# Kernel tuning notes

Measured on AMD Instinct MI355X. Metric: run time of the kernel, lower is better.

Reference implementation:

```python
import jax, jax.numpy as jnp
import numpy as np

DIM = 1024
HEADS = 16
HEAD_DIM = DIM // HEADS
BLOCK = 32
FEAT = 128
EPS = 1e-8


def setup_inputs() -> dict:
    key = jax.random.key(0)
    ks = jax.random.split(key, 5)
    b, n = 4, 4096
    x = jax.random.normal(ks[0], (b, n, DIM), dtype=jnp.float32)
    Wqkv = jax.random.normal(ks[1], (DIM, 3 * DIM), dtype=jnp.float32) / np.sqrt(DIM)
    proj = jax.random.normal(ks[2], (HEADS, HEAD_DIM, FEAT), dtype=jnp.float32) / np.sqrt(HEAD_DIM)
    Wout = jax.random.normal(ks[3], (DIM, DIM), dtype=jnp.float32) / np.sqrt(DIM)
    bout = jnp.zeros((DIM,), dtype=jnp.float32)
    return {"x": x, "Wqkv": Wqkv, "proj": proj, "Wout": Wout, "bout": bout}


def reference(x, Wqkv, proj, Wout, bout):
    b, n, d = x.shape
    h, dh = HEADS, HEAD_DIM
    nb = n // BLOCK
    qkv = x @ Wqkv                                    # [b, n, 3d]
    q, k, v = jnp.split(qkv, 3, axis=-1)
    # [b, h, nb, bs, dh]
    def to_blocks(t):
        return t.reshape(b, nb, BLOCK, h, dh).transpose(0, 3, 1, 2, 4)
    q, k, v = to_blocks(q), to_blocks(k), to_blocks(v)
    # per-head feature projection + elu feature map
    qf = jax.nn.elu(jnp.einsum('bhmsd,hdf->bhmsf', q, proj)) + 1.0
    kf = jax.nn.elu(jnp.einsum('bhmsd,hdf->bhmsf', k, proj)) + 1.0
    kv = jnp.einsum('bhmsf,bhmsd->bhmfd', kf, v)      # per-block kv state
    out = jnp.einsum('bhmsf,bhmfd->bhmsd', qf, kv)
    z = 1.0 / (jnp.einsum('bhmsf,bhmf->bhms', qf, kf.sum(axis=3)) + EPS)
    out = out * z[..., None]
    out = out.transpose(0, 2, 3, 1, 4).reshape(b, n, d)  # [b, n, d]
    return out @ Wout + bout
```

## Files before the change

### kernel.cpp

```cpp
#include <hip/hip_runtime.h>
#include <stdint.h>


typedef unsigned short u16;
typedef __attribute__((ext_vector_type(4))) float f32x4;
typedef __attribute__((ext_vector_type(8))) __bf16 bf16x8;
typedef __attribute__((ext_vector_type(8))) u16 us8;
typedef __attribute__((ext_vector_type(4))) u16 us4;

#define GLOAD_LDS16(g, l)                                                      \
  __builtin_amdgcn_global_load_lds(                                            \
      (const __attribute__((address_space(1))) void*)(g),                      \
      (__attribute__((address_space(3))) void*)(l), 16, 0, 0)

__device__ __forceinline__ u16 f2bf(float f) {
  union { float f; unsigned u; } x; x.f = f;
  return (u16)((x.u + 0x7fffu + ((x.u >> 16) & 1u)) >> 16);
}

__device__ __forceinline__ bf16x8 ld8(const void* p) {
  return __builtin_bit_cast(bf16x8, *(const us8*)p);
}

__device__ __forceinline__ f32x4 mfma16(bf16x8 a, bf16x8 b, f32x4 c) {
  return __builtin_amdgcn_mfma_f32_16x16x32_bf16(a, b, c, 0, 0, 0);
}

__global__ void cast_bf16_k(const float* __restrict__ in, u16* __restrict__ out,
                            int n4) {
  int stride = gridDim.x * blockDim.x;
  for (int i = blockIdx.x * blockDim.x + threadIdx.x; i < n4; i += stride) {
    f32x4 v = ((const f32x4*)in)[i];
    us4 o;
    o[0] = f2bf(v[0]); o[1] = f2bf(v[1]); o[2] = f2bf(v[2]); o[3] = f2bf(v[3]);
    ((us4*)out)[i] = o;
  }
}

__global__ __launch_bounds__(256)
void tcast_k(const float* __restrict__ in, u16* __restrict__ out, int R, int C) {
  __shared__ float tile[32][33];
  int tx = threadIdx.x & 31, ty = threadIdx.x >> 5;
  int r0 = blockIdx.y * 32, c0 = blockIdx.x * 32;
#pragma unroll
  for (int i = 0; i < 32; i += 8)
    tile[ty + i][tx] = in[(size_t)(r0 + ty + i) * C + c0 + tx];
  __syncthreads();
#pragma unroll
  for (int i = 0; i < 32; i += 8)
    out[(size_t)(c0 + ty + i) * R + r0 + tx] = f2bf(tile[tx][ty + i]);
}

__global__ __launch_bounds__(256)
void tcastv_k(const float* __restrict__ Wqkv, u16* __restrict__ dst) {
  __shared__ float tile[32][33];
  int tx = threadIdx.x & 31, ty = threadIdx.x >> 5;
  int e0 = blockIdx.y * 32, j0 = blockIdx.x * 32;
#pragma unroll
  for (int i = 0; i < 32; i += 8)
    tile[ty + i][tx] = Wqkv[(size_t)(e0 + ty + i) * 3072 + 2048 + j0 + tx];
  __syncthreads();
#pragma unroll
  for (int i = 0; i < 32; i += 8)
    dst[(size_t)(j0 + ty + i) * 1024 + e0 + tx] = f2bf(tile[tx][ty + i]);
}

__global__ __launch_bounds__(256)
void wqpb_k(const float* __restrict__ Wqkv, const float* __restrict__ proj,
            u16* __restrict__ Bt) {
  __shared__ float pl[64][128];
  const int ec = blockIdx.x, h = blockIdx.y, qk = blockIdx.z;
  const float* ph = proj + (size_t)h * 8192;
  for (int i = threadIdx.x; i < 2048; i += 256)
    ((f32x4*)&pl[0][0])[i] = ((const f32x4*)ph)[i];
  __syncthreads();
  const int e = ec * 128 + (threadIdx.x >> 1);
  const int f0 = (threadIdx.x & 1) * 64;
  float wrow[64];
  const float* src = Wqkv + (size_t)e * 3072 + qk * 1024 + h * 64;
#pragma unroll
  for (int i = 0; i < 16; ++i)
    *(f32x4*)&wrow[i * 4] = *(const f32x4*)&src[i * 4];
  u16* dst = Bt + (size_t)(h * 256 + qk * 128) * 1024 + e;
  for (int fg = 0; fg < 16; ++fg) {
    f32x4 acc = (f32x4){0.f, 0.f, 0.f, 0.f};
    const int f = f0 + fg * 4;
#pragma unroll
    for (int d = 0; d < 64; ++d) {
      f32x4 p = *(f32x4*)&pl[d][f];
      acc += wrow[d] * p;
    }
#pragma unroll
    for (int u = 0; u < 4; ++u) dst[(size_t)(f + u) * 1024] = f2bf(acc[u]);
  }
}

template <int EPI>
__global__ __launch_bounds__(512, 1)
void gemm8p_k(const u16* __restrict__ A, int lda,
              const u16* __restrict__ Bt, int ldb,
              const float* __restrict__ bias,
              u16* __restrict__ o_bf16, const u16* __restrict__ v_in,
              float* __restrict__ o_f32, int K, int ntx) {
  __shared__ __align__(16) char lds[131072];
  const int tid = threadIdx.x, lane = tid & 63, w = tid >> 6;
  const int wm = w >> 2, wn = w & 3;
  const int lr = lane & 15, lg = lane >> 4;
  const int cpx = (int)gridDim.x >> 3;
  const int bid = blockIdx.x;
  const int s = (bid & 7) * cpx + (bid >> 3);
  const int bxN = (s % ntx) * 256;
  const int byM = (s / ntx) * 256;
  const int nt = K >> 6;

  const int srow = w * 8 + (lane >> 3);
  const int scol = ((lane & 7) ^ ((lane >> 3) & 7)) * 8;

  auto stg = [&](const u16* src, int ld, int row0, int kt, int dstoff) {
#pragma unroll
    for (int j = 0; j < 2; ++j)
      GLOAD_LDS16(src + (size_t)(row0 + j * 64 + srow) * ld + kt + scol,
                  lds + dstoff + j * 8192 + w * 1024);
  };
  auto stgA0 = [&](int t) { stg(A, lda, byM, t * 64, (t & 1) * 65536); };
  auto stgA1 = [&](int t) { stg(A, lda, byM + 128, t * 64, (t & 1) * 65536 + 16384); };
  auto stgB0 = [&](int t) { stg(Bt, ldb, bxN, t * 64, (t & 1) * 65536 + 32768); };
  auto stgB1 = [&](int t) { stg(Bt, ldb, bxN + 128, t * 64, (t & 1) * 65536 + 49152); };

  f32x4 acc[8][4];
#pragma unroll
  for (int i = 0; i < 8; ++i)
#pragma unroll
    for (int j = 0; j < 4; ++j) acc[i][j] = (f32x4){0.f, 0.f, 0.f, 0.f};

  stgA0(0); stgA1(0); stgB0(0); stgB1(0);
  if (nt > 1) {
    stgB0(1); stgB1(1);
    asm volatile("s_waitcnt vmcnt(4)" ::: "memory");
  } else {
    asm volatile("s_waitcnt vmcnt(0)" ::: "memory");
  }
  __builtin_amdgcn_s_barrier();

  for (int t = 0; t < nt; ++t) {
    const char* Ab = lds + (t & 1) * 65536 + wm * 16384;
    const char* Bb = lds + (t & 1) * 65536 + 32768 + (wn >> 1) * 16384;
    const int brow = (wn & 1) * 64;
    bf16x8 alo[4][2], ahi[4][2], bl[4][2];

    if (t + 1 < nt) { stgA0(t + 1); stgA1(t + 1); }
#pragma unroll
    for (int i = 0; i < 4; ++i)
#pragma unroll
      for (int ks = 0; ks < 2; ++ks) {
        int row = i * 16 + lr;
        alo[i][ks] = ld8(Ab + row * 128 + ((ks * 64 + lg * 16) ^ ((row & 7) << 4)));
      }
#pragma unroll
    for (int j = 0; j < 4; ++j)
#pragma unroll
      for (int ks = 0; ks < 2; ++ks) {
        int row = brow + j * 16 + lr;
        bl[j][ks] = ld8(Bb + row * 128 + ((ks * 64 + lg * 16) ^ ((row & 7) << 4)));
      }
#pragma unroll
    for (int i = 0; i < 4; ++i)
#pragma unroll
      for (int j = 0; j < 4; ++j)
#pragma unroll
        for (int ks = 0; ks < 2; ++ks)
          acc[i][j] = mfma16(alo[i][ks], bl[j][ks], acc[i][j]);
    __builtin_amdgcn_s_barrier();

    if (t + 2 < nt) { stgB0(t + 2); stgB1(t + 2); }
#pragma unroll
    for (int i = 0; i < 4; ++i)
#pragma unroll
      for (int ks = 0; ks < 2; ++ks) {
        int row = (4 + i) * 16 + lr;
        ahi[i][ks] = ld8(Ab + row * 128 + ((ks * 64 + lg * 16) ^ ((row & 7) << 4)));
      }
#pragma unroll
    for (int i = 0; i < 4; ++i)
#pragma unroll
      for (int j = 0; j < 4; ++j)
#pragma unroll
        for (int ks = 0; ks < 2; ++ks)
          acc[4 + i][j] = mfma16(ahi[i][ks], bl[j][ks], acc[4 + i][j]);
    if (t < nt - 2)
      asm volatile("s_waitcnt vmcnt(4)" ::: "memory");
    else
      asm volatile("s_waitcnt vmcnt(0)" ::: "memory");
    __builtin_amdgcn_s_barrier();
  }

  if (EPI == 1) {
#pragma unroll
    for (int mi = 0; mi < 8; ++mi)
#pragma unroll
      for (int nj = 0; nj < 4; ++nj) {
        const int col = bxN + wn * 64 + nj * 16 + lr;
        const float bia = bias[col];
#pragma unroll
        for (int rr = 0; rr < 4; ++rr) {
          const int row = byM + wm * 128 + mi * 16 + lg * 4 + rr;
          o_f32[(size_t)row * 1024 + col] = acc[mi][nj][rr] + bia;
        }
      }
    return;
  }

  const int hh = bxN >> 8;

  us8 vreg[4];
  if (EPI == 0) {
    const u16* vrow = v_in +
        (size_t)(byM + w * 32 + (lane >> 1)) * 1024 + hh * 64 + (lane & 1) * 32;
#pragma unroll
    for (int c = 0; c < 4; ++c) vreg[c] = *(const us8*)&vrow[c * 8];
  }

  u16* cl = (u16*)lds;
#pragma unroll
  for (int mi = 0; mi < 8; ++mi)
#pragma unroll
    for (int nj = 0; nj < 4; ++nj)
#pragma unroll
      for (int rr = 0; rr < 4; ++rr) {
        const int rl = wm * 128 + mi * 16 + lg * 4 + rr;
        const int clm = wn * 64 + nj * 16 + lr;
        float xv = acc[mi][nj][rr];
        float v = (EPI == 0) ? (xv > 0.f ? xv + 1.f : __expf(xv)) : xv;
        *(u16*)((char*)cl + ((rl * 512 + clm * 2) ^ ((rl & 7) << 4))) = f2bf(v);
      }
  __syncthreads();

  if (EPI == 2) {
#pragma unroll
    for (int it = 0; it < 16; ++it) {
      const int chunk = it * 512 + tid;
      const int r = chunk >> 5, k = chunk & 31;
      us8 val = *(us8*)((char*)cl + ((r * 512 + k * 16) ^ ((r & 7) << 4)));
      *(us8*)&o_bf16[(size_t)(byM + r) * 1024 + bxN + k * 8] = val;
    }
    return;
  }

  char* sw = (char*)lds + w * 16384;

  f32x4 sacc[2][2];
#pragma unroll
  for (int mm = 0; mm < 2; ++mm)
#pragma unroll
    for (int nn = 0; nn < 2; ++nn) sacc[mm][nn] = (f32x4){0.f, 0.f, 0.f, 0.f};
#pragma unroll
  for (int ks = 0; ks < 4; ++ks) {
    bf16x8 aq[2], bk[2];
#pragma unroll
    for (int mm = 0; mm < 2; ++mm) {
      const int row = mm * 16 + lr;
      aq[mm] = ld8(sw + ((row * 512 + ks * 64 + lg * 16) ^ ((row & 7) << 4)));
      bk[mm] = ld8(sw + ((row * 512 + 256 + ks * 64 + lg * 16) ^ ((row & 7) << 4)));
    }
#pragma unroll
    for (int mm = 0; mm < 2; ++mm)
#pragma unroll
      for (int nn = 0; nn < 2; ++nn)
        sacc[mm][nn] = mfma16(aq[mm], bk[nn], sacc[mm][nn]);
  }

  float rs[2][4];
#pragma unroll
  for (int mm = 0; mm < 2; ++mm)
#pragma unroll
    for (int r = 0; r < 4; ++r) {
      float tv = sacc[mm][0][r] + sacc[mm][1][r];
      tv += __shfl_xor(tv, 1);
      tv += __shfl_xor(tv, 2);
      tv += __shfl_xor(tv, 4);
      tv += __shfl_xor(tv, 8);
      rs[mm][r] = tv;
    }

#pragma unroll
  for (int mm = 0; mm < 2; ++mm)
#pragma unroll
    for (int nn = 0; nn < 2; ++nn)
#pragma unroll
      for (int r = 0; r < 4; ++r) {
        const int row = mm * 16 + lg * 4 + r;
        *(u16*)(sw + row * 64 + (((nn * 16 + lr) * 2) ^ ((row & 3) << 4))) =
            f2bf(sacc[mm][nn][r]);
      }

#pragma unroll
  for (int c = 0; c < 4; ++c)
    *(us8*)(sw + 2048 + (lane >> 1) * 144 + (lane & 1) * 64 + c * 16) = vreg[c];
  const u16* V_l = (const u16*)(sw + 2048);
  bf16x8 vfr[4];
#pragma unroll
  for (int nn = 0; nn < 4; ++nn) {
    us8 g;
#pragma unroll
    for (int j = 0; j < 8; ++j) g[j] = V_l[(lg * 8 + j) * 72 + nn * 16 + lr];
    vfr[nn] = __builtin_bit_cast(bf16x8, g);
  }

  f32x4 pacc[2][4];
#pragma unroll
  for (int mm = 0; mm < 2; ++mm)
#pragma unroll
    for (int nn = 0; nn < 4; ++nn) pacc[mm][nn] = (f32x4){0.f, 0.f, 0.f, 0.f};
#pragma unroll
  for (int mm = 0; mm < 2; ++mm) {
    const int row = mm * 16 + lr;
    bf16x8 a = ld8(sw + row * 64 + ((lg * 16) ^ ((row & 3) << 4)));
#pragma unroll
    for (int nn = 0; nn < 4; ++nn) pacc[mm][nn] = mfma16(a, vfr[nn], pacc[mm][nn]);
  }

#pragma unroll
  for (int mm = 0; mm < 2; ++mm)
#pragma unroll
    for (int r = 0; r < 4; ++r) {
      const float z = 1.f / (rs[mm][r] + 1e-8f);
      const int row = mm * 16 + lg * 4 + r;
#pragma unroll
      for (int nn = 0; nn < 4; ++nn)
        *(u16*)(sw + 8192 + row * 128 + (nn * 16 + lr) * 2) =
            f2bf(pacc[mm][nn][r] * z);
    }
  u16* orow = o_bf16 +
      (size_t)(byM + w * 32 + (lane >> 1)) * 1024 + hh * 64 + (lane & 1) * 32;
#pragma unroll
  for (int c = 0; c < 4; ++c)
    *(us8*)&orow[c * 8] =
        *(us8*)(sw + 8192 + (lane >> 1) * 128 + (lane & 1) * 64 + c * 16);
}

extern "C" void kernel_launch(void* const* d_in, const int* in_sizes, int n_in,
                              void* d_out, int out_size, void* d_ws,
                              size_t ws_size, hipStream_t stream) {
  const float* x = (const float*)d_in[0];
  const float* Wqkv = (const float*)d_in[1];
  const float* proj = (const float*)d_in[2];
  const float* Wout = (const float*)d_in[3];
  const float* bout = (const float*)d_in[4];
  float* out = (float*)d_out;

  char* ws = (char*)d_ws;
  char* doc = (char*)d_out;

  u16* xb    = (u16*)doc;
  u16* btqk  = (u16*)(doc + 33554432);
  u16* wvT   = (u16*)(doc + 41943040);
  u16* vbuf  = (u16*)ws;
  u16* woutT = (u16*)(ws + 33554432);

  cast_bf16_k<<<2048, 256, 0, stream>>>(x, xb, 4194304);
  tcastv_k<<<dim3(32, 32), 256, 0, stream>>>(Wqkv, wvT);
  wqpb_k<<<dim3(8, 16, 2), 256, 0, stream>>>(Wqkv, proj, btqk);
  tcast_k<<<dim3(32, 32), 256, 0, stream>>>(Wout, woutT, 1024, 1024);

  gemm8p_k<2><<<256, 512, 0, stream>>>(xb, 1024, wvT, 1024, nullptr,
                                       vbuf, nullptr, nullptr, 1024, 4);

  gemm8p_k<0><<<1024, 512, 0, stream>>>(xb, 1024, btqk, 1024, nullptr,
                                        vbuf, vbuf, nullptr, 1024, 16);

  gemm8p_k<1><<<256, 512, 0, stream>>>(vbuf, 1024, woutT, 1024, bout,
                                       nullptr, nullptr, out, 1024, 4);
}
```

Baseline: 394.7 us.

## Merge prep kernels and switch GEMM to 4-stage BK=32 pipeline with swizzled epilogue

Fuses the four preprocessing kernels (x cast, Wv transpose-cast, Wqk·proj product, Wout transpose) into one launch dispatched by block index. The main GEMM changes from a double-buffered K=64 tile with split A-half loads to a four-buffer K=32 ring that prefetches three tiles ahead and issues one barrier per step. It also adds an XOR swizzle to the epilogue LDS staging to avoid bank conflicts. These target launch overhead, pipeline latency and LDS conflicts, at the cost of more barriers per unit of K work.

```diff
diff --git a/kernel.cpp b/kernel.cpp
--- a/kernel.cpp
+++ b/kernel.cpp
@@ -26,78 +26,76 @@
   return __builtin_amdgcn_mfma_f32_16x16x32_bf16(a, b, c, 0, 0, 0);
 }
 
-__global__ void cast_bf16_k(const float* __restrict__ in, u16* __restrict__ out,
-                            int n4) {
-  int stride = gridDim.x * blockDim.x;
-  for (int i = blockIdx.x * blockDim.x + threadIdx.x; i < n4; i += stride) {
-    f32x4 v = ((const f32x4*)in)[i];
-    us4 o;
-    o[0] = f2bf(v[0]); o[1] = f2bf(v[1]); o[2] = f2bf(v[2]); o[3] = f2bf(v[3]);
-    ((us4*)out)[i] = o;
-  }
-}
-
 __global__ __launch_bounds__(256)
-void tcast_k(const float* __restrict__ in, u16* __restrict__ out, int R, int C) {
-  __shared__ float tile[32][33];
-  int tx = threadIdx.x & 31, ty = threadIdx.x >> 5;
-  int r0 = blockIdx.y * 32, c0 = blockIdx.x * 32;
-#pragma unroll
-  for (int i = 0; i < 32; i += 8)
-    tile[ty + i][tx] = in[(size_t)(r0 + ty + i) * C + c0 + tx];
-  __syncthreads();
-#pragma unroll
-  for (int i = 0; i < 32; i += 8)
-    out[(size_t)(c0 + ty + i) * R + r0 + tx] = f2bf(tile[tx][ty + i]);
-}
-
-__global__ __launch_bounds__(256)
-void tcastv_k(const float* __restrict__ Wqkv, u16* __restrict__ dst) {
-  __shared__ float tile[32][33];
-  int tx = threadIdx.x & 31, ty = threadIdx.x >> 5;
-  int e0 = blockIdx.y * 32, j0 = blockIdx.x * 32;
-#pragma unroll
-  for (int i = 0; i < 32; i += 8)
-    tile[ty + i][tx] = Wqkv[(size_t)(e0 + ty + i) * 3072 + 2048 + j0 + tx];
-  __syncthreads();
-#pragma unroll
-  for (int i = 0; i < 32; i += 8)
-    dst[(size_t)(j0 + ty + i) * 1024 + e0 + tx] = f2bf(tile[tx][ty + i]);
-}
-
-__global__ __launch_bounds__(256)
-void wqpb_k(const float* __restrict__ Wqkv, const float* __restrict__ proj,
-            u16* __restrict__ Bt) {
-  __shared__ float pl[64][128];
-  const int ec = blockIdx.x, h = blockIdx.y, qk = blockIdx.z;
-  const float* ph = proj + (size_t)h * 8192;
-  for (int i = threadIdx.x; i < 2048; i += 256)
-    ((f32x4*)&pl[0][0])[i] = ((const f32x4*)ph)[i];
-  __syncthreads();
-  const int e = ec * 128 + (threadIdx.x >> 1);
-  const int f0 = (threadIdx.x & 1) * 64;
-  float wrow[64];
-  const float* src = Wqkv + (size_t)e * 3072 + qk * 1024 + h * 64;
-#pragma unroll
-  for (int i = 0; i < 16; ++i)
-    *(f32x4*)&wrow[i * 4] = *(const f32x4*)&src[i * 4];
-  u16* dst = Bt + (size_t)(h * 256 + qk * 128) * 1024 + e;
-  for (int fg = 0; fg < 16; ++fg) {
-    f32x4 acc = (f32x4){0.f, 0.f, 0.f, 0.f};
-    const int f = f0 + fg * 4;
-#pragma unroll
-    for (int d = 0; d < 64; ++d) {
-      f32x4 p = *(f32x4*)&pl[d][f];
-      acc += wrow[d] * p;
-    }
-#pragma unroll
-    for (int u = 0; u < 4; ++u) dst[(size_t)(f + u) * 1024] = f2bf(acc[u]);
+void prep_k(const float* __restrict__ x, const float* __restrict__ Wqkv,
+            const float* __restrict__ proj, const float* __restrict__ Wout,
+            u16* __restrict__ xb, u16* __restrict__ wvT,
+            u16* __restrict__ btqk, u16* __restrict__ woutT) {
+  __shared__ __align__(16) float smem[8192 + 64];
+  const int b = blockIdx.x, tid = threadIdx.x;
+
+  if (b < 2048) {
+    const int stride = 2048 * 256;
+    for (int i = b * 256 + tid; i < 4194304; i += stride) {
+      f32x4 v = ((const f32x4*)x)[i];
+      us4 o;
+      o[0] = f2bf(v[0]); o[1] = f2bf(v[1]); o[2] = f2bf(v[2]); o[3] = f2bf(v[3]);
+      ((us4*)xb)[i] = o;
+    }
+  } else if (b < 3072) {
+    float (&tile)[32][33] = *reinterpret_cast<float (*)[32][33]>(smem);
+    const int idx = b - 2048;
+    const int j0 = (idx & 31) * 32, e0 = (idx >> 5) * 32;
+    const int tx = tid & 31, ty = tid >> 5;
+#pragma unroll
+    for (int i = 0; i < 32; i += 8)
+      tile[ty + i][tx] = Wqkv[(size_t)(e0 + ty + i) * 3072 + 2048 + j0 + tx];
+    __syncthreads();
+#pragma unroll
+    for (int i = 0; i < 32; i += 8)
+      wvT[(size_t)(j0 + ty + i) * 1024 + e0 + tx] = f2bf(tile[tx][ty + i]);
+  } else if (b < 3328) {
+    float (&pl)[64][128] = *reinterpret_cast<float (*)[64][128]>(smem);
+    const int idx = b - 3072;
+    const int ec = idx & 7, h = (idx >> 3) & 15, qk = idx >> 7;
+    const float* ph = proj + (size_t)h * 8192;
+    for (int i = tid; i < 2048; i += 256)
+      ((f32x4*)&pl[0][0])[i] = ((const f32x4*)ph)[i];
+    __syncthreads();
+    const int e = ec * 128 + (tid >> 1);
+    const int f0 = (tid & 1) * 64;
+    float wrow[64];
+    const float* src = Wqkv + (size_t)e * 3072 + qk * 1024 + h * 64;
+#pragma unroll
+    for (int i = 0; i < 16; ++i)
+      *(f32x4*)&wrow[i * 4] = *(const f32x4*)&src[i * 4];
+    u16* dst = btqk + (size_t)(h * 256 + qk * 128) * 1024 + e;
+    for (int fg = 0; fg < 16; ++fg) {
+      f32x4 acc = (f32x4){0.f, 0.f, 0.f, 0.f};
+      const int f = f0 + fg * 4;
+#pragma unroll
+      for (int d = 0; d < 64; ++d) acc += wrow[d] * *(f32x4*)&pl[d][f];
+#pragma unroll
+      for (int u = 0; u < 4; ++u) dst[(size_t)(f + u) * 1024] = f2bf(acc[u]);
+    }
+  } else {
+    float (&tile)[32][33] = *reinterpret_cast<float (*)[32][33]>(smem);
+    const int idx = b - 3328;
+    const int c0 = (idx & 31) * 32, r0 = (idx >> 5) * 32;
+    const int tx = tid & 31, ty = tid >> 5;
+#pragma unroll
+    for (int i = 0; i < 32; i += 8)
+      tile[ty + i][tx] = Wout[(size_t)(r0 + ty + i) * 1024 + c0 + tx];
+    __syncthreads();
+#pragma unroll
+    for (int i = 0; i < 32; i += 8)
+      woutT[(size_t)(c0 + ty + i) * 1024 + r0 + tx] = f2bf(tile[tx][ty + i]);
   }
 }
 
 template <int EPI>
 __global__ __launch_bounds__(512, 1)
-void gemm8p_k(const u16* __restrict__ A, int lda,
+void gemm4b_k(const u16* __restrict__ A, int lda,
               const u16* __restrict__ Bt, int ldb,
               const float* __restrict__ bias,
               u16* __restrict__ o_bf16, const u16* __restrict__ v_in,
@@ -111,21 +109,22 @@
   const int s = (bid & 7) * cpx + (bid >> 3);
   const int bxN = (s % ntx) * 256;
   const int byM = (s / ntx) * 256;
-  const int nt = K >> 6;
-
-  const int srow = w * 8 + (lane >> 3);
-  const int scol = ((lane & 7) ^ ((lane >> 3) & 7)) * 8;
-
-  auto stg = [&](const u16* src, int ld, int row0, int kt, int dstoff) {
-#pragma unroll
-    for (int j = 0; j < 2; ++j)
-      GLOAD_LDS16(src + (size_t)(row0 + j * 64 + srow) * ld + kt + scol,
-                  lds + dstoff + j * 8192 + w * 1024);
+  const int nt = K >> 5;
+
+  const int r_s = tid >> 2;
+  const int scol = ((tid & 3) ^ ((r_s & 3) ^ ((r_s >> 2) & 1))) * 8;
+
+  auto stage_tile = [&](int t) {
+    const int kt = t * 32, bo = (t & 3) * 32768;
+    GLOAD_LDS16(A + (size_t)(byM + r_s) * lda + kt + scol,
+                lds + bo + w * 1024);
+    GLOAD_LDS16(A + (size_t)(byM + 128 + r_s) * lda + kt + scol,
+                lds + bo + 8192 + w * 1024);
+    GLOAD_LDS16(Bt + (size_t)(bxN + r_s) * ldb + kt + scol,
+                lds + bo + 16384 + w * 1024);
+    GLOAD_LDS16(Bt + (size_t)(bxN + 128 + r_s) * ldb + kt + scol,
+                lds + bo + 24576 + w * 1024);
   };
-  auto stgA0 = [&](int t) { stg(A, lda, byM, t * 64, (t & 1) * 65536); };
-  auto stgA1 = [&](int t) { stg(A, lda, byM + 128, t * 64, (t & 1) * 65536 + 16384); };
-  auto stgB0 = [&](int t) { stg(Bt, ldb, bxN, t * 64, (t & 1) * 65536 + 32768); };
-  auto stgB1 = [&](int t) { stg(Bt, ldb, bxN + 128, t * 64, (t & 1) * 65536 + 49152); };
 
   f32x4 acc[8][4];
 #pragma unroll
@@ -133,61 +132,32 @@
 #pragma unroll
     for (int j = 0; j < 4; ++j) acc[i][j] = (f32x4){0.f, 0.f, 0.f, 0.f};
 
-  stgA0(0); stgA1(0); stgB0(0); stgB1(0);
-  if (nt > 1) {
-    stgB0(1); stgB1(1);
-    asm volatile("s_waitcnt vmcnt(4)" ::: "memory");
-  } else {
-    asm volatile("s_waitcnt vmcnt(0)" ::: "memory");
-  }
+  stage_tile(0); stage_tile(1); stage_tile(2);
+  asm volatile("s_waitcnt vmcnt(8)" ::: "memory");
   __builtin_amdgcn_s_barrier();
 
   for (int t = 0; t < nt; ++t) {
-    const char* Ab = lds + (t & 1) * 65536 + wm * 16384;
-    const char* Bb = lds + (t & 1) * 65536 + 32768 + (wn >> 1) * 16384;
-    const int brow = (wn & 1) * 64;
-    bf16x8 alo[4][2], ahi[4][2], bl[4][2];
-
-    if (t + 1 < nt) { stgA0(t + 1); stgA1(t + 1); }
-#pragma unroll
-    for (int i = 0; i < 4; ++i)
-#pragma unroll
-      for (int ks = 0; ks < 2; ++ks) {
-        int row = i * 16 + lr;
-        alo[i][ks] = ld8(Ab + row * 128 + ((ks * 64 + lg * 16) ^ ((row & 7) << 4)));
-      }
-#pragma unroll
-    for (int j = 0; j < 4; ++j)
-#pragma unroll
-      for (int ks = 0; ks < 2; ++ks) {
-        int row = brow + j * 16 + lr;
-        bl[j][ks] = ld8(Bb + row * 128 + ((ks * 64 + lg * 16) ^ ((row & 7) << 4)));
-      }
-#pragma unroll
-    for (int i = 0; i < 4; ++i)
-#pragma unroll
-      for (int j = 0; j < 4; ++j)
-#pragma unroll
-        for (int ks = 0; ks < 2; ++ks)
-          acc[i][j] = mfma16(alo[i][ks], bl[j][ks], acc[i][j]);
-    __builtin_amdgcn_s_barrier();
-
-    if (t + 2 < nt) { stgB0(t + 2); stgB1(t + 2); }
-#pragma unroll
-    for (int i = 0; i < 4; ++i)
-#pragma unroll
-      for (int ks = 0; ks < 2; ++ks) {
-        int row = (4 + i) * 16 + lr;
-        ahi[i][ks] = ld8(Ab + row * 128 + ((ks * 64 + lg * 16) ^ ((row & 7) << 4)));
-      }
-#pragma unroll
-    for (int i = 0; i < 4; ++i)
-#pragma unroll
-      for (int j = 0; j < 4; ++j)
-#pragma unroll
-        for (int ks = 0; ks < 2; ++ks)
-          acc[4 + i][j] = mfma16(ahi[i][ks], bl[j][ks], acc[4 + i][j]);
-    if (t < nt - 2)
+    if (t + 3 < nt) stage_tile(t + 3);
+    const char* bufp = lds + (t & 3) * 32768;
+    bf16x8 bfr[4];
+#pragma unroll
+    for (int nj = 0; nj < 4; ++nj) {
+      const int rb = wn * 64 + nj * 16 + lr;
+      bfr[nj] = ld8(bufp + 16384 + rb * 64 +
+                    ((lg * 16) ^ ((((rb & 3) ^ ((rb >> 2) & 1))) << 4)));
+    }
+#pragma unroll
+    for (int mi = 0; mi < 8; ++mi) {
+      const int ra = wm * 128 + mi * 16 + lr;
+      bf16x8 a = ld8(bufp + ra * 64 +
+                     ((lg * 16) ^ ((((ra & 3) ^ ((ra >> 2) & 1))) << 4)));
+#pragma unroll
+      for (int nj = 0; nj < 4; ++nj)
+        acc[mi][nj] = mfma16(a, bfr[nj], acc[mi][nj]);
+    }
+    if (t < nt - 3)
+      asm volatile("s_waitcnt vmcnt(8)" ::: "memory");
+    else if (t == nt - 3)
       asm volatile("s_waitcnt vmcnt(4)" ::: "memory");
     else
       asm volatile("s_waitcnt vmcnt(0)" ::: "memory");
@@ -327,15 +297,18 @@
       const int row = mm * 16 + lg * 4 + r;
 #pragma unroll
       for (int nn = 0; nn < 4; ++nn)
-        *(u16*)(sw + 8192 + row * 128 + (nn * 16 + lr) * 2) =
+        *(u16*)(sw + 8192 + row * 128 +
+                (((nn * 16 + lr) * 2) ^ ((row & 7) << 4))) =
             f2bf(pacc[mm][nn][r] * z);
     }
   u16* orow = o_bf16 +
       (size_t)(byM + w * 32 + (lane >> 1)) * 1024 + hh * 64 + (lane & 1) * 32;
+  const int vr = lane >> 1;
 #pragma unroll
   for (int c = 0; c < 4; ++c)
     *(us8*)&orow[c * 8] =
-        *(us8*)(sw + 8192 + (lane >> 1) * 128 + (lane & 1) * 64 + c * 16);
+        *(us8*)(sw + 8192 + vr * 128 +
+                (((lane & 1) * 64 + c * 16) ^ ((vr & 7) << 4)));
 }
 
 extern "C" void kernel_launch(void* const* d_in, const int* in_sizes, int n_in,
@@ -357,17 +330,14 @@
   u16* vbuf  = (u16*)ws;
   u16* woutT = (u16*)(ws + 33554432);
 
-  cast_bf16_k<<<2048, 256, 0, stream>>>(x, xb, 4194304);
-  tcastv_k<<<dim3(32, 32), 256, 0, stream>>>(Wqkv, wvT);
-  wqpb_k<<<dim3(8, 16, 2), 256, 0, stream>>>(Wqkv, proj, btqk);
-  tcast_k<<<dim3(32, 32), 256, 0, stream>>>(Wout, woutT, 1024, 1024);
-
-  gemm8p_k<2><<<256, 512, 0, stream>>>(xb, 1024, wvT, 1024, nullptr,
+  prep_k<<<4352, 256, 0, stream>>>(x, Wqkv, proj, Wout, xb, wvT, btqk, woutT);
+
+  gemm4b_k<2><<<256, 512, 0, stream>>>(xb, 1024, wvT, 1024, nullptr,
                                        vbuf, nullptr, nullptr, 1024, 4);
 
-  gemm8p_k<0><<<1024, 512, 0, stream>>>(xb, 1024, btqk, 1024, nullptr,
+  gemm4b_k<0><<<1024, 512, 0, stream>>>(xb, 1024, btqk, 1024, nullptr,
                                         vbuf, vbuf, nullptr, 1024, 16);
 
-  gemm8p_k<1><<<256, 512, 0, stream>>>(vbuf, 1024, woutT, 1024, bout,
+  gemm4b_k<1><<<256, 512, 0, stream>>>(vbuf, 1024, woutT, 1024, bout,
                                        nullptr, nullptr, out, 1024, 4);
 }
```

New measurement: 421.3 us. 6.8% more time.
